# Performance work log

Measured on AMD Instinct MI355X. Metric: run time of the kernel, lower is better.

The kernel has to match this reference:

```python
import jax, jax.numpy as jnp
import numpy as np

B, T, D, H, TE = 8, 1024, 1024, 16, 2048  # batch, seq, latent_dim, heads, time_embed_dim
LN_EPS = 1e-5


def layer_norm(x, w, b):
    m = jnp.mean(x, axis=-1, keepdims=True)
    v = jnp.var(x, axis=-1, keepdims=True)
    return (x - m) / jnp.sqrt(v + LN_EPS) * w + b


def setup_inputs() -> dict:
    key = jax.random.key(0)
    ks = jax.random.split(key, 8)
    s = lambda k, sh: (jax.random.normal(k, sh, jnp.float32) * 0.02)
    return dict(
        x=jax.random.normal(ks[0], (B, T, D), jnp.float32),
        emb=jax.random.normal(ks[1], (B, TE), jnp.float32),
        src_mask=jnp.ones((B, T), jnp.float32),
        norm_w=jnp.ones((D,), jnp.float32), norm_b=jnp.zeros((D,), jnp.float32),
        q_w=s(ks[2], (D, D)), q_b=jnp.zeros((D,), jnp.float32),
        k_w=s(ks[3], (D, D)), k_b=jnp.zeros((D,), jnp.float32),
        v_w=s(ks[4], (D, D)), v_b=jnp.zeros((D,), jnp.float32),
        emb_w=s(ks[5], (TE, 2 * D)), emb_b=jnp.zeros((2 * D,), jnp.float32),
        sb_norm_w=jnp.ones((D,), jnp.float32), sb_norm_b=jnp.zeros((D,), jnp.float32),
        out_w=s(ks[6], (D, D)), out_b=jnp.zeros((D,), jnp.float32),
    )


def reference(x, emb, src_mask, norm_w, norm_b, q_w, q_b, k_w, k_b, v_w, v_b,
              emb_w, emb_b, sb_norm_w, sb_norm_b, out_w, out_b):
    Bx, Tx, Dx = x.shape
    # the torch module applies the SAME LayerNorm to x three times; compute once
    xn = layer_norm(x, norm_w, norm_b)                      # [B,T,D]
    q = (xn @ q_w + q_b).reshape(Bx, Tx, H, -1)             # [B,T,H,l]
    k = (xn @ k_w + k_b).reshape(Bx, Tx, H, -1)
    att = jnp.einsum('bnhl,bmhl->bnmh', q, k)               # [B,T,T,H] (no 1/sqrt(d) scaling, as in source)
    mask = src_mask.reshape(Bx, 1, Tx, 1)
    att = att + (1.0 - mask) * -1000000.0
    att = jax.nn.softmax(att, axis=2)                       # softmax over keys (dim m)
    v = ((xn @ v_w + v_b) * src_mask[:, :, None]).reshape(Bx, Tx, H, -1)
    y = jnp.einsum('bnmh,bmhl->bnhl', att, v).reshape(Bx, Tx, Dx)
    # StylizationBlock (dropout is identity in eval)
    e = jax.nn.silu(emb) @ emb_w + emb_b                    # [B,2D]
    scale, shift = jnp.split(e[:, None, :], 2, axis=2)      # each [B,1,D]
    h = layer_norm(y, sb_norm_w, sb_norm_b) * (1.0 + scale) + shift
    h = jax.nn.silu(h) @ out_w + out_b
    return x + h
```

## Files before the change

kernel.cpp:

```cpp
#include <hip/hip_runtime.h>
#include <cstddef>
#include <cstdint>

#define B_SZ 8
#define T_SEQ 1024
#define D_MODEL 1024
#define NH 16
#define HD 64
#define TE_DIM 2048
#define BT_ROWS 8192

typedef short bf16x8 __attribute__((ext_vector_type(8)));
typedef float f32x4 __attribute__((ext_vector_type(4)));

#define MFMA16(a, b, c) __builtin_amdgcn_mfma_f32_16x16x32_bf16(a, b, c, 0, 0, 0)
#define EXP2(x) __builtin_amdgcn_exp2f(x)

__device__ inline unsigned short f2b(float f) {
  union { float f; unsigned u; } v; v.f = f;
  unsigned r = v.u + 0x7FFF + ((v.u >> 16) & 1);
  return (unsigned short)(r >> 16);
}

__device__ inline float b2f(unsigned short u) {
  union { unsigned u; float f; } v; v.u = ((unsigned)u) << 16; return v.f;
}

__device__ inline unsigned cvtpk(float a, float b) {
  unsigned r;
  asm("v_cvt_pk_bf16_f32 %0, %1, %2" : "=v"(r) : "v"(a), "v"(b));
  return r;
}

__device__ inline float max3f(float a, float b, float c) {
  return fmaxf(fmaxf(a, b), c);
}

__device__ inline void gll16(const void* g, void* l) {
  __builtin_amdgcn_global_load_lds(
      (const __attribute__((address_space(1))) unsigned int*)g,
      (__attribute__((address_space(3))) unsigned int*)l, 16, 0, 0);
}

__global__ __launch_bounds__(256) void prep_kernel(
    const float* __restrict__ x, const float* __restrict__ norm_w,
    const float* __restrict__ norm_b, unsigned short* __restrict__ xn,
    const float* __restrict__ s0, const float* __restrict__ s1,
    const float* __restrict__ s2, const float* __restrict__ s3,
    unsigned short* __restrict__ d0, unsigned short* __restrict__ d1,
    unsigned short* __restrict__ d2, unsigned short* __restrict__ d3)
{
  __shared__ float red[8];
  __shared__ float sT[32][33];
  int bid = blockIdx.x;
  int tid = threadIdx.x;
  if (bid < BT_ROWS) {
    int row = bid;
    const float* xr = x + (size_t)row * D_MODEL;
    float4 xv = *(const float4*)&xr[tid * 4];
    float s  = xv.x + xv.y + xv.z + xv.w;
    float ss = xv.x*xv.x + xv.y*xv.y + xv.z*xv.z + xv.w*xv.w;
    #pragma unroll
    for (int off = 32; off; off >>= 1) {
      s  += __shfl_xor(s, off);
      ss += __shfl_xor(ss, off);
    }
    int wv = tid >> 6;
    if ((tid & 63) == 0) { red[wv] = s; red[4 + wv] = ss; }
    __syncthreads();
    s  = red[0] + red[1] + red[2] + red[3];
    ss = red[4] + red[5] + red[6] + red[7];
    float mean = s * (1.f / D_MODEL);
    float var  = ss * (1.f / D_MODEL) - mean * mean;
    float inv  = rsqrtf(var + 1e-5f);
    float4 w4 = *(const float4*)&norm_w[tid * 4];
    float4 b4 = *(const float4*)&norm_b[tid * 4];
    ushort4 o;
    o.x = f2b((xv.x - mean) * inv * w4.x + b4.x);
    o.y = f2b((xv.y - mean) * inv * w4.y + b4.y);
    o.z = f2b((xv.z - mean) * inv * w4.z + b4.z);
    o.w = f2b((xv.w - mean) * inv * w4.w + b4.w);
    int kg = tid >> 4, cb = (tid >> 1) & 7, e = (tid & 1) * 4;
    int col = kg * 64 + ((cb ^ (row & 7)) * 8) + e;
    *(ushort4*)&xn[(size_t)row * D_MODEL + col] = o;
  } else {
    int tb = bid - BT_ROWS;
    int z = tb >> 10, yy = (tb >> 5) & 31, xx = tb & 31;
    const float* in = z == 0 ? s0 : z == 1 ? s1 : z == 2 ? s2 : s3;
    unsigned short* out = z == 0 ? d0 : z == 1 ? d1 : z == 2 ? d2 : d3;
    int tx = tid & 31, ty = tid >> 5;
    int r0 = yy * 32, c0 = xx * 32;
    #pragma unroll
    for (int rr = 0; rr < 4; ++rr)
      sT[ty + rr * 8][tx] = in[(size_t)(r0 + ty + rr * 8) * D_MODEL + c0 + tx];
    __syncthreads();
    int k = r0 + tx;
    int kg = k >> 6, cb = (k >> 3) & 7, e = k & 7;
    #pragma unroll
    for (int rr = 0; rr < 4; ++rr) {
      int n = c0 + ty + rr * 8;
      int col = kg * 64 + ((cb ^ (n & 7)) * 8) + e;
      out[(size_t)n * D_MODEL + col] = f2b(sT[tx][ty + rr * 8]);
    }
  }
}

__global__ __launch_bounds__(512, 2) void gemm_qkv8(
    const unsigned short* __restrict__ A, const unsigned short* __restrict__ W,
    const float* __restrict__ b0, const float* __restrict__ b1,
    const float* __restrict__ b2, const float* __restrict__ mask,
    unsigned short* __restrict__ O,
    const float* __restrict__ emb, const float* __restrict__ emb_w,
    float* __restrict__ partial)
{
  const int K = 1024;
  __shared__ __align__(16) unsigned short SA[3][256 * 64];
  __shared__ __align__(16) unsigned short SB[3][128 * 64];
  int tid = threadIdx.x;
  int bid = blockIdx.x;

  if (bid >= 768) {
    int kb = bid - 768;
    float* ses = (float*)&SA[0][0];
    int t0 = kb * 32;
    if (tid < 256) {
      int b = tid >> 5, t = tid & 31;
      float v = emb[b * TE_DIM + t0 + t];
      ses[b * 32 + t] = v / (1.f + __expf(-v));
    }
    __syncthreads();
    int n = tid * 4;
    f32x4 acc[B_SZ];
    #pragma unroll
    for (int b = 0; b < B_SZ; ++b) acc[b] = (f32x4){0.f, 0.f, 0.f, 0.f};
    #pragma unroll 4
    for (int t = 0; t < 32; ++t) {
      f32x4 wv = *(const f32x4*)&emb_w[(size_t)(t0 + t) * (2 * D_MODEL) + n];
      #pragma unroll
      for (int b = 0; b < B_SZ; ++b) {
        float s = ses[b * 32 + t];
        acc[b][0] = fmaf(s, wv[0], acc[b][0]);
        acc[b][1] = fmaf(s, wv[1], acc[b][1]);
        acc[b][2] = fmaf(s, wv[2], acc[b][2]);
        acc[b][3] = fmaf(s, wv[3], acc[b][3]);
      }
    }
    #pragma unroll
    for (int b = 0; b < B_SZ; ++b)
      *(f32x4*)&partial[((size_t)kb * B_SZ + b) * (2 * D_MODEL) + n] = acc[b];
    return;
  }

  int wid = tid >> 6, lane = tid & 63, g = lane >> 4, lq = lane & 15;
  int wm = wid >> 1, wn = wid & 1;
  int xcd = bid & 7, ii = bid >> 3;
  int mt = xcd * 4 + (ii & 3), nt = ii >> 2;
  int m0 = mt * 256;
  int wg = nt >> 3;
  int n0 = (nt & 7) * 128;
  const unsigned short* Bt = W + ((size_t)wg << 20);
  const float* bias = wg == 0 ? b0 : wg == 1 ? b1 : b2;

  f32x4 acc[4][4];
  #pragma unroll
  for (int i = 0; i < 4; ++i)
    #pragma unroll
    for (int j = 0; j < 4; ++j)
      acc[i][j] = (f32x4){0.f, 0.f, 0.f, 0.f};

  const unsigned short* aSrc = A + (size_t)(m0 + (tid >> 3)) * K + (tid & 7) * 8;
  const unsigned short* bSrc = Bt + (size_t)(n0 + (tid >> 3)) * K + (tid & 7) * 8;

  #define STAGE8(slot, t)                                                      \
    {                                                                          \
      size_t ko = (size_t)(t) * 64;                                            \
      _Pragma("unroll")                                                        \
      for (int i2 = 0; i2 < 4; ++i2)                                           \
        gll16(aSrc + ko + (size_t)i2 * 64 * K,                                 \
              (char*)&SA[slot][0] + tid * 16 + i2 * 8192);                     \
      _Pragma("unroll")                                                        \
      for (int i2 = 0; i2 < 2; ++i2)                                           \
        gll16(bSrc + ko + (size_t)i2 * 64 * K,                                 \
              (char*)&SB[slot][0] + tid * 16 + i2 * 8192);                     \
    }

  STAGE8(0, 0)
  STAGE8(1, 1)
  asm volatile("s_waitcnt vmcnt(6)" ::: "memory");
  asm volatile("s_barrier" ::: "memory");

  int cA0 = (g ^ (lq & 7)) * 16;
  int cA1 = ((4 + g) ^ (lq & 7)) * 16;

  #pragma unroll
  for (int t = 0; t < 16; ++t) {
    const char* sa = (const char*)&SA[t % 3][0];
    const char* sb = (const char*)&SB[t % 3][0];
    bf16x8 af[4][2], bf[4][2];
    #pragma unroll
    for (int i = 0; i < 4; ++i) {
      int ra = wm * 64 + i * 16 + lq;
      af[i][0] = *(const bf16x8*)(sa + ra * 128 + cA0);
      af[i][1] = *(const bf16x8*)(sa + ra * 128 + cA1);
      int rb = wn * 64 + i * 16 + lq;
      bf[i][0] = *(const bf16x8*)(sb + rb * 128 + cA0);
      bf[i][1] = *(const bf16x8*)(sb + rb * 128 + cA1);
    }
    if (t < 14) {
      STAGE8((t + 2) % 3, t + 2)
      asm volatile("s_waitcnt vmcnt(6)" ::: "memory");
    } else if (t == 14) {
      asm volatile("s_waitcnt vmcnt(0)" ::: "memory");
    }
    __builtin_amdgcn_s_setprio(1);
    #pragma unroll
    for (int i = 0; i < 4; ++i)
      #pragma unroll
      for (int j = 0; j < 4; ++j) {
        acc[i][j] = MFMA16(af[i][0], bf[j][0], acc[i][j]);
        acc[i][j] = MFMA16(af[i][1], bf[j][1], acc[i][j]);
      }
    __builtin_amdgcn_s_setprio(0);
    if (t < 15) asm volatile("s_barrier" ::: "memory");
  }
  #undef STAGE8

  int colbase = n0 + wn * 64;
  #pragma unroll
  for (int i = 0; i < 4; ++i) {
    int mrow0 = m0 + wm * 64 + i * 16 + g * 4;
    #pragma unroll
    for (int j = 0; j < 4; ++j) {
      int n = colbase + j * 16 + lq;
      float bv = bias[n];
      int h = n >> 6, dd = n & 63;
      if (wg < 2) {
        float scale = wg == 0 ? 1.44269504f : 1.0f;
        unsigned short* Cb = O + ((size_t)wg << 23);
        #pragma unroll
        for (int rr = 0; rr < 4; ++rr) {
          int m = mrow0 + rr;
          int b = m >> 10, tt = m & 1023;
          Cb[((size_t)((b * NH + h) * T_SEQ + tt)) * HD + dd] = f2b((acc[i][j][rr] + bv) * scale);
        }
      } else {
        unsigned short* Cb = O + ((size_t)2 << 23);
        int b = mrow0 >> 10, tt = mrow0 & 1023;
        ushort4 pk;
        unsigned short* pp = (unsigned short*)&pk;
        #pragma unroll
        for (int rr = 0; rr < 4; ++rr)
          pp[rr] = f2b((acc[i][j][rr] + bv) * mask[mrow0 + rr]);
        *(ushort4*)&Cb[((size_t)((b * NH + h) * HD + dd)) * T_SEQ + tt] = pk;
      }
    }
  }
}

__global__ __launch_bounds__(256) void gemm_out(
    const unsigned short* __restrict__ A, const unsigned short* __restrict__ Bt,
    const float* __restrict__ bias, const float* __restrict__ resid,
    float* __restrict__ C)
{
  const int K = 1024;
  __shared__ __align__(16) unsigned short As[128 * 64];
  __shared__ __align__(16) unsigned short Bs[128 * 64];
  int l = blockIdx.x;
  int xcd = l & 7, ii = l >> 3;
  int mt = xcd * 8 + (ii & 7), nt = ii >> 3;
  int m0 = mt * 128, n0 = nt * 128;

  int tid = threadIdx.x;
  int lane = tid & 63, w = tid >> 6;
  int g = lane >> 4, lq = lane & 15;
  int wr = w >> 1, wc = w & 1;
  f32x4 acc[4][4];
  #pragma unroll
  for (int i = 0; i < 4; ++i)
    #pragma unroll
    for (int j = 0; j < 4; ++j)
      acc[i][j] = (f32x4){0.f, 0.f, 0.f, 0.f};

  const unsigned short* aSrc = A + (size_t)(m0 + (tid >> 3)) * K + (tid & 7) * 8;
  const unsigned short* bSrc = Bt + (size_t)(n0 + (tid >> 3)) * K + (tid & 7) * 8;
  char* aDst = (char*)As + tid * 16;
  char* bDst = (char*)Bs + tid * 16;

  for (int k0 = 0; k0 < K; k0 += 64) {
    #pragma unroll
    for (int it = 0; it < 4; ++it) {
      gll16(aSrc + k0 + it * 32 * K, aDst + it * 4096);
      gll16(bSrc + k0 + it * 32 * K, bDst + it * 4096);
    }
    __syncthreads();
    #pragma unroll
    for (int kh = 0; kh < 2; ++kh) {
      bf16x8 af[4], bfr[4];
      #pragma unroll
      for (int i = 0; i < 4; ++i) {
        int ra = wr * 64 + i * 16 + lq;
        af[i] = *(const bf16x8*)((const char*)As + ra * 128 + (((kh * 4 + g) ^ (ra & 7)) * 16));
        int rb = wc * 64 + i * 16 + lq;
        bfr[i] = *(const bf16x8*)((const char*)Bs + rb * 128 + (((kh * 4 + g) ^ (rb & 7)) * 16));
      }
      #pragma unroll
      for (int i = 0; i < 4; ++i)
        #pragma unroll
        for (int j = 0; j < 4; ++j)
          acc[i][j] = MFMA16(af[i], bfr[j], acc[i][j]);
    }
    __syncthreads();
  }

  int colbase = n0 + wc * 64;
  #pragma unroll
  for (int i = 0; i < 4; ++i) {
    int mrow0 = m0 + wr * 64 + i * 16 + g * 4;
    #pragma unroll
    for (int j = 0; j < 4; ++j) {
      int n = colbase + j * 16 + lq;
      float bv = bias[n];
      #pragma unroll
      for (int rr = 0; rr < 4; ++rr) {
        int m = mrow0 + rr;
        C[(size_t)m * D_MODEL + n] = acc[i][j][rr] + bv + resid[(size_t)m * D_MODEL + n];
      }
    }
  }
}

__global__ __launch_bounds__(256, 2) void attn_mfma7(
    const unsigned short* __restrict__ Q, const unsigned short* __restrict__ K,
    const unsigned short* __restrict__ Vt, const float* __restrict__ mask,
    unsigned short* __restrict__ y,
    const float* __restrict__ partial, const float* __restrict__ emb_b,
    float* __restrict__ e)
{
  __shared__ __align__(16) unsigned short SM[32768];
  int tid = threadIdx.x;
  int bid = blockIdx.x;

  if (bid >= 512) {
    int idx = (bid - 512) * 256 + tid;
    int b = idx >> 11, n = idx & 2047;
    float acc = emb_b[n];
    #pragma unroll 8
    for (int kb = 0; kb < 64; ++kb)
      acc += partial[((size_t)kb * B_SZ + b) * (2 * D_MODEL) + n];
    e[b * (2 * D_MODEL) + n] = acc;
    return;
  }

  unsigned short* Kb = SM;
  unsigned short* Vb = SM + 8192;
  unsigned short* Pb = SM + 16384;

  int w = tid >> 6, lane = tid & 63;
  int g = lane >> 4, lq = lane & 15;
  int lid = (bid & 7) * 64 + (bid >> 3);
  int qb = lid & 3, h = (lid >> 2) & 15, b = lid >> 6;
  int q0 = qb * 256 + w * 64;
  size_t hb = ((size_t)(b * NH + h)) * T_SEQ * HD;

  bf16x8 bq[4][2];
  #pragma unroll
  for (int qa = 0; qa < 4; ++qa)
    #pragma unroll
    for (int kh = 0; kh < 2; ++kh)
      bq[qa][kh] = *(const bf16x8*)(Q + hb + (size_t)(q0 + qa * 16 + lq) * HD + kh * 32 + g * 8);

  bf16x8 ones;
  #pragma unroll
  for (int i = 0; i < 8; ++i) ones[i] = (short)16256;

  const char* kBase = (const char*)(K + hb) + lq * 128 + g * 16;
  const char* vBase = (const char*)(Vt + hb) + lq * 2048 + g * 16;
  int c0 = 2 * w, c1 = 2 * w + 1;
  const char* kS0 = kBase + (c0 >> 1) * 2048 + (c0 & 1) * 64;
  const char* kS1 = kBase + (c1 >> 1) * 2048 + (c1 & 1) * 64;
  const char* vS0 = vBase + (c0 >> 1) * 32768 + (c0 & 1) * 64;
  const char* vS1 = vBase + (c1 >> 1) * 32768 + (c1 & 1) * 64;

  f32x4 o[4][4];
  f32x4 osum[4];
  #pragma unroll
  for (int qa = 0; qa < 4; ++qa) {
    osum[qa] = (f32x4){0.f, 0.f, 0.f, 0.f};
    #pragma unroll
    for (int dt = 0; dt < 4; ++dt)
      o[dt][qa] = (f32x4){0.f, 0.f, 0.f, 0.f};
  }
  float mrun[4] = {-3.0e38f, -3.0e38f, -3.0e38f, -3.0e38f};
  const float* maskb = mask + b * T_SEQ;

  gll16(kS0, Kb + c0 * 512);
  gll16(kS1, Kb + c1 * 512);
  gll16(vS0, Vb + c0 * 512);
  gll16(vS1, Vb + c1 * 512);
  __syncthreads();

  for (int t = 0; t < 16; ++t) {
    int cur = t & 1;
    int kv0 = t * 64;
    if (t < 15) {
      int nxt = cur ^ 1;
      size_t ko = (size_t)(kv0 + 64) * 128;
      size_t vo = (size_t)(kv0 + 64) * 2;
      gll16(kS0 + ko, Kb + nxt * 4096 + c0 * 512);
      gll16(kS1 + ko, Kb + nxt * 4096 + c1 * 512);
      gll16(vS0 + vo, Vb + nxt * 4096 + c0 * 512);
      gll16(vS1 + vo, Vb + nxt * 4096 + c1 * 512);
    }
    const unsigned short* Kc = Kb + cur * 4096;
    const unsigned short* Vc = Vb + cur * 4096;

    f32x4 mbv[4];
    #pragma unroll
    for (int kt = 0; kt < 4; ++kt) {
      float4 mk = *(const float4*)&maskb[kv0 + kt * 16 + g * 4];
      mbv[kt][0] = fmaf(mk.x, 1500000.f, -1500000.f);
      mbv[kt][1] = fmaf(mk.y, 1500000.f, -1500000.f);
      mbv[kt][2] = fmaf(mk.z, 1500000.f, -1500000.f);
      mbv[kt][3] = fmaf(mk.w, 1500000.f, -1500000.f);
    }

    bf16x8 kf[4][2];
    #pragma unroll
    for (int kt = 0; kt < 4; ++kt)
      #pragma unroll
      for (int kh = 0; kh < 2; ++kh)
        kf[kt][kh] = *(const bf16x8*)(Kc + (kt * 2 + kh) * 512 + lane * 8);

    f32x4 st[4][4];
    __builtin_amdgcn_s_setprio(1);
    #pragma unroll
    for (int kt = 0; kt < 4; ++kt)
      #pragma unroll
      for (int qa = 0; qa < 4; ++qa) {
        st[kt][qa] = MFMA16(kf[kt][0], bq[qa][0], mbv[kt]);
        st[kt][qa] = MFMA16(kf[kt][1], bq[qa][1], st[kt][qa]);
      }
    __builtin_amdgcn_s_setprio(0);

    bf16x8 vf[4][2];
    #pragma unroll
    for (int dt = 0; dt < 4; ++dt)
      #pragma unroll
      for (int kh = 0; kh < 2; ++kh)
        vf[dt][kh] = *(const bf16x8*)(Vc + (dt * 2 + kh) * 512 + lane * 8);

    float tmax[4];
    #pragma unroll
    for (int qa = 0; qa < 4; ++qa) {
      float m0v = max3f(st[0][qa][0], st[0][qa][1], st[0][qa][2]);
      float m1v = max3f(st[0][qa][3], st[1][qa][0], st[1][qa][1]);
      float m2v = max3f(st[1][qa][2], st[1][qa][3], st[2][qa][0]);
      float m3v = max3f(st[2][qa][1], st[2][qa][2], st[2][qa][3]);
      float m4v = max3f(st[3][qa][0], st[3][qa][1], st[3][qa][2]);
      float t0v = max3f(m0v, m1v, st[3][qa][3]);
      float t1v = max3f(m2v, m3v, m4v);
      float tm = fmaxf(t0v, t1v);
      tm = fmaxf(tm, __shfl_xor(tm, 16));
      tm = fmaxf(tm, __shfl_xor(tm, 32));
      tmax[qa] = tm;
    }
    bool need = false;
    #pragma unroll
    for (int qa = 0; qa < 4; ++qa) need = need || (tmax[qa] > mrun[qa] + 11.5f);
    if (__any((int)need)) {
      #pragma unroll
      for (int qa = 0; qa < 4; ++qa) {
        float mnew = fmaxf(mrun[qa], tmax[qa]);
        float corr = EXP2(mrun[qa] - mnew);
        osum[qa][0] *= corr; osum[qa][1] *= corr;
        osum[qa][2] *= corr; osum[qa][3] *= corr;
        #pragma unroll
        for (int dt = 0; dt < 4; ++dt) {
          o[dt][qa][0] *= corr; o[dt][qa][1] *= corr;
          o[dt][qa][2] *= corr; o[dt][qa][3] *= corr;
        }
        mrun[qa] = mnew;
      }
    }
    #pragma unroll
    for (int qa = 0; qa < 4; ++qa)
      #pragma unroll
      for (int kt = 0; kt < 4; ++kt)
        #pragma unroll
        for (int r = 0; r < 4; ++r)
          st[kt][qa][r] = EXP2(st[kt][qa][r] - mrun[qa]);

    #pragma unroll
    for (int qa = 0; qa < 4; ++qa) {
      unsigned short* Pq = Pb + (w * 4 + qa) * 1024;
      #pragma unroll
      for (int kt = 0; kt < 4; ++kt) {
        uint2 pk2;
        pk2.x = cvtpk(st[kt][qa][0], st[kt][qa][1]);
        pk2.y = cvtpk(st[kt][qa][2], st[kt][qa][3]);
        *(uint2*)((char*)Pq + lq * 128 +
                  (((kt * 2 + (g >> 1)) ^ (lq & 7)) * 16) + (g & 1) * 8) = pk2;
      }
    }

    __builtin_amdgcn_s_setprio(1);
    #pragma unroll
    for (int qa = 0; qa < 4; ++qa) {
      const unsigned short* Pq = Pb + (w * 4 + qa) * 1024;
      #pragma unroll
      for (int kh = 0; kh < 2; ++kh) {
        bf16x8 pa = *(const bf16x8*)((const char*)Pq + lq * 128 +
                                     (((kh * 4 + g) ^ (lq & 7)) * 16));
        osum[qa] = MFMA16(ones, pa, osum[qa]);
        #pragma unroll
        for (int dt = 0; dt < 4; ++dt)
          o[dt][qa] = MFMA16(vf[dt][kh], pa, o[dt][qa]);
      }
    }
    __builtin_amdgcn_s_setprio(0);

    __syncthreads();
  }

  unsigned short* sc = SM + w * 4096;
  #pragma unroll
  for (int qa = 0; qa < 4; ++qa) {
    float inv = 1.f / osum[qa][0];
    #pragma unroll
    for (int dt = 0; dt < 4; ++dt) {
      uint2 pk;
      pk.x = cvtpk(o[dt][qa][0] * inv, o[dt][qa][1] * inv);
      pk.y = cvtpk(o[dt][qa][2] * inv, o[dt][qa][3] * inv);
      *(uint2*)(sc + (qa * 16 + lq) * 64 + dt * 16 + g * 4) = pk;
    }
  }
  #pragma unroll
  for (int it = 0; it < 16; ++it) {
    int row = it * 4 + g;
    ushort4 v = *(const ushort4*)(sc + row * 64 + lq * 4);
    *(ushort4*)&y[(size_t)(b * T_SEQ + q0 + row) * D_MODEL + h * HD + lq * 4] = v;
  }
}

__global__ __launch_bounds__(256) void ln2_kernel(
    const unsigned short* __restrict__ y, const float* __restrict__ w,
    const float* __restrict__ b, const float* __restrict__ e,
    unsigned short* __restrict__ gout)
{
  __shared__ float red[8];
  int row = blockIdx.x;
  int tid = threadIdx.x;
  int bb = row >> 10;
  ushort4 u = *(const ushort4*)&y[(size_t)row * D_MODEL + tid * 4];
  float4 yv = {b2f(u.x), b2f(u.y), b2f(u.z), b2f(u.w)};
  float s  = yv.x + yv.y + yv.z + yv.w;
  float ss = yv.x*yv.x + yv.y*yv.y + yv.z*yv.z + yv.w*yv.w;
  #pragma unroll
  for (int off = 32; off; off >>= 1) {
    s  += __shfl_xor(s, off);
    ss += __shfl_xor(ss, off);
  }
  int wv = tid >> 6;
  if ((tid & 63) == 0) { red[wv] = s; red[4 + wv] = ss; }
  __syncthreads();
  s  = red[0] + red[1] + red[2] + red[3];
  ss = red[4] + red[5] + red[6] + red[7];
  float mean = s * (1.f / D_MODEL);
  float var  = ss * (1.f / D_MODEL) - mean * mean;
  float inv  = rsqrtf(var + 1e-5f);
  float vals[4] = {yv.x, yv.y, yv.z, yv.w};
  ushort4 o;
  unsigned short* op = (unsigned short*)&o;
  #pragma unroll
  for (int j = 0; j < 4; j++) {
    int c = tid * 4 + j;
    float val = (vals[j] - mean) * inv * w[c] + b[c];
    float sc = e[bb * (2 * D_MODEL) + c];
    float sh = e[bb * (2 * D_MODEL) + D_MODEL + c];
    val = val * (1.f + sc) + sh;
    op[j] = f2b(val / (1.f + __expf(-val)));
  }
  int kg = tid >> 4, cb = (tid >> 1) & 7, ee = (tid & 1) * 4;
  int col = kg * 64 + ((cb ^ (row & 7)) * 8) + ee;
  *(ushort4*)&gout[(size_t)row * D_MODEL + col] = o;
}

extern "C" void kernel_launch(void* const* d_in, const int* in_sizes, int n_in,
                              void* d_out, int out_size, void* d_ws, size_t ws_size,
                              hipStream_t stream) {
  const float* x      = (const float*)d_in[0];
  const float* emb    = (const float*)d_in[1];
  const float* mask   = (const float*)d_in[2];
  const float* norm_w = (const float*)d_in[3];
  const float* norm_b = (const float*)d_in[4];
  const float* q_w    = (const float*)d_in[5];
  const float* q_b    = (const float*)d_in[6];
  const float* k_w    = (const float*)d_in[7];
  const float* k_b    = (const float*)d_in[8];
  const float* v_w    = (const float*)d_in[9];
  const float* v_b    = (const float*)d_in[10];
  const float* emb_w  = (const float*)d_in[11];
  const float* emb_b  = (const float*)d_in[12];
  const float* sb_w   = (const float*)d_in[13];
  const float* sb_b   = (const float*)d_in[14];
  const float* out_w  = (const float*)d_in[15];
  const float* out_b  = (const float*)d_in[16];
  float* out = (float*)d_out;

  char* ws = (char*)d_ws;
  const size_t MB = 1u << 20;
  unsigned short* xn   = (unsigned short*)(ws);
  unsigned short* qkv  = (unsigned short*)(ws + 16 * MB);
  unsigned short* qb   = qkv;
  unsigned short* kb   = qkv + (1u << 23);
  unsigned short* vt   = qkv + (2u << 23);
  unsigned short* yb   = (unsigned short*)(ws + 64 * MB);
  unsigned short* gb   = (unsigned short*)(ws + 96 * MB);
  float*          ep   = (float*)(ws + 96 * MB);
  unsigned short* w3t  = (unsigned short*)(ws + 112 * MB);
  unsigned short* owt  = (unsigned short*)(ws + 118 * MB);
  float*          eb   = (float*)(ws + 120 * MB);

  prep_kernel<<<BT_ROWS + 4096, 256, 0, stream>>>(
      x, norm_w, norm_b, xn,
      q_w, k_w, v_w, out_w,
      w3t, w3t + (1u << 20), w3t + (2u << 20), owt);

  gemm_qkv8<<<832, 512, 0, stream>>>(xn, w3t, q_b, k_b, v_b, mask, qkv,
                                     emb, emb_w, ep);

  attn_mfma7<<<576, 256, 0, stream>>>(qb, kb, vt, mask, yb, ep, emb_b, eb);

  ln2_kernel<<<BT_ROWS, 256, 0, stream>>>(yb, sb_w, sb_b, eb, gb);

  gemm_out<<<512, 256, 0, stream>>>(gb, owt, out_b, x, out);
}
```

Baseline: 180.7 us.

## Move emb projection into prep kernel and split attention across 8 waves

New measurement: 203.6 us. 12.6% more time.

```diff
diff --git a/kernel.cpp b/kernel.cpp
--- a/kernel.cpp
+++ b/kernel.cpp
@@ -48,10 +48,13 @@
     const float* __restrict__ s0, const float* __restrict__ s1,
     const float* __restrict__ s2, const float* __restrict__ s3,
     unsigned short* __restrict__ d0, unsigned short* __restrict__ d1,
-    unsigned short* __restrict__ d2, unsigned short* __restrict__ d3)
+    unsigned short* __restrict__ d2, unsigned short* __restrict__ d3,
+    const float* __restrict__ emb, const float* __restrict__ emb_w,
+    float* __restrict__ partial)
 {
   __shared__ float red[8];
   __shared__ float sT[32][33];
+  __shared__ float ses[B_SZ][32];
   int bid = blockIdx.x;
   int tid = threadIdx.x;
   if (bid < BT_ROWS) {
@@ -83,7 +86,7 @@
     int kg = tid >> 4, cb = (tid >> 1) & 7, e = (tid & 1) * 4;
     int col = kg * 64 + ((cb ^ (row & 7)) * 8) + e;
     *(ushort4*)&xn[(size_t)row * D_MODEL + col] = o;
-  } else {
+  } else if (bid < BT_ROWS + 4096) {
     int tb = bid - BT_ROWS;
     int z = tb >> 10, yy = (tb >> 5) & 31, xx = tb & 31;
     const float* in = z == 0 ? s0 : z == 1 ? s1 : z == 2 ? s2 : s3;
@@ -102,6 +105,35 @@
       int col = kg * 64 + ((cb ^ (n & 7)) * 8) + e;
       out[(size_t)n * D_MODEL + col] = f2b(sT[tx][ty + rr * 8]);
     }
+  } else {
+    int tb2 = bid - (BT_ROWS + 4096);
+    int colb = tb2 & 1, kb = tb2 >> 1;
+    int t0 = kb * 32;
+    {
+      int b = tid >> 5, t = tid & 31;
+      float v = emb[b * TE_DIM + t0 + t];
+      ses[b][t] = v / (1.f + __expf(-v));
+    }
+    __syncthreads();
+    int n = colb * 1024 + tid * 4;
+    f32x4 acc[B_SZ];
+    #pragma unroll
+    for (int b = 0; b < B_SZ; ++b) acc[b] = (f32x4){0.f, 0.f, 0.f, 0.f};
+    #pragma unroll 4
+    for (int t = 0; t < 32; ++t) {
+      f32x4 wv = *(const f32x4*)&emb_w[(size_t)(t0 + t) * (2 * D_MODEL) + n];
+      #pragma unroll
+      for (int b = 0; b < B_SZ; ++b) {
+        float s = ses[b][t];
+        acc[b][0] = fmaf(s, wv[0], acc[b][0]);
+        acc[b][1] = fmaf(s, wv[1], acc[b][1]);
+        acc[b][2] = fmaf(s, wv[2], acc[b][2]);
+        acc[b][3] = fmaf(s, wv[3], acc[b][3]);
+      }
+    }
+    #pragma unroll
+    for (int b = 0; b < B_SZ; ++b)
+      *(f32x4*)&partial[((size_t)kb * B_SZ + b) * (2 * D_MODEL) + n] = acc[b];
   }
 }
 
@@ -109,50 +141,15 @@
     const unsigned short* __restrict__ A, const unsigned short* __restrict__ W,
     const float* __restrict__ b0, const float* __restrict__ b1,
     const float* __restrict__ b2, const float* __restrict__ mask,
-    unsigned short* __restrict__ O,
-    const float* __restrict__ emb, const float* __restrict__ emb_w,
-    float* __restrict__ partial)
+    unsigned short* __restrict__ O)
 {
   const int K = 1024;
   __shared__ __align__(16) unsigned short SA[3][256 * 64];
   __shared__ __align__(16) unsigned short SB[3][128 * 64];
   int tid = threadIdx.x;
-  int bid = blockIdx.x;
-
-  if (bid >= 768) {
-    int kb = bid - 768;
-    float* ses = (float*)&SA[0][0];
-    int t0 = kb * 32;
-    if (tid < 256) {
-      int b = tid >> 5, t = tid & 31;
-      float v = emb[b * TE_DIM + t0 + t];
-      ses[b * 32 + t] = v / (1.f + __expf(-v));
-    }
-    __syncthreads();
-    int n = tid * 4;
-    f32x4 acc[B_SZ];
-    #pragma unroll
-    for (int b = 0; b < B_SZ; ++b) acc[b] = (f32x4){0.f, 0.f, 0.f, 0.f};
-    #pragma unroll 4
-    for (int t = 0; t < 32; ++t) {
-      f32x4 wv = *(const f32x4*)&emb_w[(size_t)(t0 + t) * (2 * D_MODEL) + n];
-      #pragma unroll
-      for (int b = 0; b < B_SZ; ++b) {
-        float s = ses[b * 32 + t];
-        acc[b][0] = fmaf(s, wv[0], acc[b][0]);
-        acc[b][1] = fmaf(s, wv[1], acc[b][1]);
-        acc[b][2] = fmaf(s, wv[2], acc[b][2]);
-        acc[b][3] = fmaf(s, wv[3], acc[b][3]);
-      }
-    }
-    #pragma unroll
-    for (int b = 0; b < B_SZ; ++b)
-      *(f32x4*)&partial[((size_t)kb * B_SZ + b) * (2 * D_MODEL) + n] = acc[b];
-    return;
-  }
-
   int wid = tid >> 6, lane = tid & 63, g = lane >> 4, lq = lane & 15;
   int wm = wid >> 1, wn = wid & 1;
+  int bid = blockIdx.x;
   int xcd = bid & 7, ii = bid >> 3;
   int mt = xcd * 4 + (ii & 3), nt = ii >> 2;
   int m0 = mt * 256;
@@ -329,7 +326,7 @@
   }
 }
 
-__global__ __launch_bounds__(256, 2) void attn_mfma7(
+__global__ __launch_bounds__(512, 2) void attn_mfma8(
     const unsigned short* __restrict__ Q, const unsigned short* __restrict__ K,
     const unsigned short* __restrict__ Vt, const float* __restrict__ mask,
     unsigned short* __restrict__ y,
@@ -341,7 +338,7 @@
   int bid = blockIdx.x;
 
   if (bid >= 512) {
-    int idx = (bid - 512) * 256 + tid;
+    int idx = (bid - 512) * 512 + tid;
     int b = idx >> 11, n = idx & 2047;
     float acc = emb_b[n];
     #pragma unroll 8
@@ -359,12 +356,12 @@
   int g = lane >> 4, lq = lane & 15;
   int lid = (bid & 7) * 64 + (bid >> 3);
   int qb = lid & 3, h = (lid >> 2) & 15, b = lid >> 6;
-  int q0 = qb * 256 + w * 64;
+  int q0 = qb * 256 + w * 32;
   size_t hb = ((size_t)(b * NH + h)) * T_SEQ * HD;
 
-  bf16x8 bq[4][2];
-  #pragma unroll
-  for (int qa = 0; qa < 4; ++qa)
+  bf16x8 bq[2][2];
+  #pragma unroll
+  for (int qa = 0; qa < 2; ++qa)
     #pragma unroll
     for (int kh = 0; kh < 2; ++kh)
       bq[qa][kh] = *(const bf16x8*)(Q + hb + (size_t)(q0 + qa * 16 + lq) * HD + kh * 32 + g * 8);
@@ -375,28 +372,23 @@
 
   const char* kBase = (const char*)(K + hb) + lq * 128 + g * 16;
   const char* vBase = (const char*)(Vt + hb) + lq * 2048 + g * 16;
-  int c0 = 2 * w, c1 = 2 * w + 1;
-  const char* kS0 = kBase + (c0 >> 1) * 2048 + (c0 & 1) * 64;
-  const char* kS1 = kBase + (c1 >> 1) * 2048 + (c1 & 1) * 64;
-  const char* vS0 = vBase + (c0 >> 1) * 32768 + (c0 & 1) * 64;
-  const char* vS1 = vBase + (c1 >> 1) * 32768 + (c1 & 1) * 64;
-
-  f32x4 o[4][4];
-  f32x4 osum[4];
-  #pragma unroll
-  for (int qa = 0; qa < 4; ++qa) {
+  const char* kSw = kBase + (w >> 1) * 2048 + (w & 1) * 64;
+  const char* vSw = vBase + (w >> 1) * 32768 + (w & 1) * 64;
+
+  f32x4 o[4][2];
+  f32x4 osum[2];
+  #pragma unroll
+  for (int qa = 0; qa < 2; ++qa) {
     osum[qa] = (f32x4){0.f, 0.f, 0.f, 0.f};
     #pragma unroll
     for (int dt = 0; dt < 4; ++dt)
       o[dt][qa] = (f32x4){0.f, 0.f, 0.f, 0.f};
   }
-  float mrun[4] = {-3.0e38f, -3.0e38f, -3.0e38f, -3.0e38f};
+  float mrun[2] = {-3.0e38f, -3.0e38f};
   const float* maskb = mask + b * T_SEQ;
 
-  gll16(kS0, Kb + c0 * 512);
-  gll16(kS1, Kb + c1 * 512);
-  gll16(vS0, Vb + c0 * 512);
-  gll16(vS1, Vb + c1 * 512);
+  gll16(kSw, Kb + w * 512);
+  gll16(vSw, Vb + w * 512);
   __syncthreads();
 
   for (int t = 0; t < 16; ++t) {
@@ -406,10 +398,8 @@
       int nxt = cur ^ 1;
       size_t ko = (size_t)(kv0 + 64) * 128;
       size_t vo = (size_t)(kv0 + 64) * 2;
-      gll16(kS0 + ko, Kb + nxt * 4096 + c0 * 512);
-      gll16(kS1 + ko, Kb + nxt * 4096 + c1 * 512);
-      gll16(vS0 + vo, Vb + nxt * 4096 + c0 * 512);
-      gll16(vS1 + vo, Vb + nxt * 4096 + c1 * 512);
+      gll16(kSw + ko, Kb + nxt * 4096 + w * 512);
+      gll16(vSw + vo, Vb + nxt * 4096 + w * 512);
     }
     const unsigned short* Kc = Kb + cur * 4096;
     const unsigned short* Vc = Vb + cur * 4096;
@@ -431,12 +421,12 @@
       for (int kh = 0; kh < 2; ++kh)
         kf[kt][kh] = *(const bf16x8*)(Kc + (kt * 2 + kh) * 512 + lane * 8);
 
-    f32x4 st[4][4];
+    f32x4 st[4][2];
     __builtin_amdgcn_s_setprio(1);
     #pragma unroll
     for (int kt = 0; kt < 4; ++kt)
       #pragma unroll
-      for (int qa = 0; qa < 4; ++qa) {
+      for (int qa = 0; qa < 2; ++qa) {
         st[kt][qa] = MFMA16(kf[kt][0], bq[qa][0], mbv[kt]);
         st[kt][qa] = MFMA16(kf[kt][1], bq[qa][1], st[kt][qa]);
       }
@@ -449,9 +439,9 @@
       for (int kh = 0; kh < 2; ++kh)
         vf[dt][kh] = *(const bf16x8*)(Vc + (dt * 2 + kh) * 512 + lane * 8);
 
-    float tmax[4];
-    #pragma unroll
-    for (int qa = 0; qa < 4; ++qa) {
+    float tmax[2];
+    #pragma unroll
+    for (int qa = 0; qa < 2; ++qa) {
       float m0v = max3f(st[0][qa][0], st[0][qa][1], st[0][qa][2]);
       float m1v = max3f(st[0][qa][3], st[1][qa][0], st[1][qa][1]);
       float m2v = max3f(st[1][qa][2], st[1][qa][3], st[2][qa][0]);
@@ -464,12 +454,10 @@
       tm = fmaxf(tm, __shfl_xor(tm, 32));
       tmax[qa] = tm;
     }
-    bool need = false;
-    #pragma unroll
-    for (int qa = 0; qa < 4; ++qa) need = need || (tmax[qa] > mrun[qa] + 11.5f);
+    bool need = (tmax[0] > mrun[0] + 11.5f) || (tmax[1] > mrun[1] + 11.5f);
     if (__any((int)need)) {
       #pragma unroll
-      for (int qa = 0; qa < 4; ++qa) {
+      for (int qa = 0; qa < 2; ++qa) {
         float mnew = fmaxf(mrun[qa], tmax[qa]);
         float corr = EXP2(mrun[qa] - mnew);
         osum[qa][0] *= corr; osum[qa][1] *= corr;
@@ -483,7 +471,7 @@
       }
     }
     #pragma unroll
-    for (int qa = 0; qa < 4; ++qa)
+    for (int qa = 0; qa < 2; ++qa)
       #pragma unroll
       for (int kt = 0; kt < 4; ++kt)
         #pragma unroll
@@ -491,8 +479,8 @@
           st[kt][qa][r] = EXP2(st[kt][qa][r] - mrun[qa]);
 
     #pragma unroll
-    for (int qa = 0; qa < 4; ++qa) {
-      unsigned short* Pq = Pb + (w * 4 + qa) * 1024;
+    for (int qa = 0; qa < 2; ++qa) {
+      unsigned short* Pq = Pb + (w * 2 + qa) * 1024;
       #pragma unroll
       for (int kt = 0; kt < 4; ++kt) {
         uint2 pk2;
@@ -505,8 +493,8 @@
 
     __builtin_amdgcn_s_setprio(1);
     #pragma unroll
-    for (int qa = 0; qa < 4; ++qa) {
-      const unsigned short* Pq = Pb + (w * 4 + qa) * 1024;
+    for (int qa = 0; qa < 2; ++qa) {
+      const unsigned short* Pq = Pb + (w * 2 + qa) * 1024;
       #pragma unroll
       for (int kh = 0; kh < 2; ++kh) {
         bf16x8 pa = *(const bf16x8*)((const char*)Pq + lq * 128 +
@@ -522,9 +510,9 @@
     __syncthreads();
   }
 
-  unsigned short* sc = SM + w * 4096;
-  #pragma unroll
-  for (int qa = 0; qa < 4; ++qa) {
+  unsigned short* sc = SM + w * 2048;
+  #pragma unroll
+  for (int qa = 0; qa < 2; ++qa) {
     float inv = 1.f / osum[qa][0];
     #pragma unroll
     for (int dt = 0; dt < 4; ++dt) {
@@ -535,7 +523,7 @@
     }
   }
   #pragma unroll
-  for (int it = 0; it < 16; ++it) {
+  for (int it = 0; it < 8; ++it) {
     int row = it * 4 + g;
     ushort4 v = *(const ushort4*)(sc + row * 64 + lq * 4);
     *(ushort4*)&y[(size_t)(b * T_SEQ + q0 + row) * D_MODEL + h * HD + lq * 4] = v;
@@ -621,15 +609,15 @@
   unsigned short* owt  = (unsigned short*)(ws + 118 * MB);
   float*          eb   = (float*)(ws + 120 * MB);
 
-  prep_kernel<<<BT_ROWS + 4096, 256, 0, stream>>>(
+  prep_kernel<<<BT_ROWS + 4096 + 128, 256, 0, stream>>>(
       x, norm_w, norm_b, xn,
       q_w, k_w, v_w, out_w,
-      w3t, w3t + (1u << 20), w3t + (2u << 20), owt);
-
-  gemm_qkv8<<<832, 512, 0, stream>>>(xn, w3t, q_b, k_b, v_b, mask, qkv,
-                                     emb, emb_w, ep);
-
-  attn_mfma7<<<576, 256, 0, stream>>>(qb, kb, vt, mask, yb, ep, emb_b, eb);
+      w3t, w3t + (1u << 20), w3t + (2u << 20), owt,
+      emb, emb_w, ep);
+
+  gemm_qkv8<<<768, 512, 0, stream>>>(xn, w3t, q_b, k_b, v_b, mask, qkv);
+
+  attn_mfma8<<<544, 512, 0, stream>>>(qb, kb, vt, mask, yb, ep, emb_b, eb);
 
   ln2_kernel<<<BT_ROWS, 256, 0, stream>>>(yb, sb_w, sb_b, eb, gb);
 
```
